# Kernel optimization log

Hardware: AMD Instinct MI355X
Metric: run time of the kernel (lower is better)

Reference implementation:

```python
import jax, jax.numpy as jnp
import numpy as np

B, C, H, W = 8, 64, 256, 256  # H must equal W (matmul shape constraint in original)


def setup_inputs() -> dict:
    key = jax.random.key(0)
    ks = jax.random.split(key, 7)
    s = 1.0 / np.sqrt(C)  # fan-in scaled init, like conv default scale
    return {
        "x": jax.random.normal(ks[0], (B, C, H, W), dtype=jnp.float32),
        "Wq": jax.random.normal(ks[1], (C, C), dtype=jnp.float32) * s,
        "bq": jax.random.normal(ks[2], (C,), dtype=jnp.float32) * s,
        "Wk": jax.random.normal(ks[3], (C, C), dtype=jnp.float32) * s,
        "bk": jax.random.normal(ks[4], (C,), dtype=jnp.float32) * s,
        "Wv": jax.random.normal(ks[5], (C, C), dtype=jnp.float32) * s,
        "bv": jax.random.normal(ks[6], (C,), dtype=jnp.float32) * s,
    }


def _conv1x1(x, Wt, b):
    # 1x1 Conv2d == per-pixel GEMM over channels: [o,c] x [b,c,h,w] -> [b,o,h,w]
    return jnp.einsum("oc,bchw->bohw", Wt, x) + b[None, :, None, None]


def reference(x, Wq, bq, Wk, bk, Wv, bv):
    q = _conv1x1(x, Wq, bq)
    k = _conv1x1(x, Wk, bk)
    v = _conv1x1(x, Wv, bv)
    # attn[b,c,i,j] = sum_h q[b,c,h,i] * k[b,c,h,j]   (q^T @ k over spatial)
    attn = jnp.einsum("bchi,bchj->bcij", q, k)
    # softmax over the CHANNEL axis (dim=-3 in torch == axis 1 here)
    attn = jax.nn.softmax(attn, axis=1)
    # out[b,c,i,j] = sum_m attn[b,c,i,m] * v[b,c,m,j]  (requires H == W)
    out = jnp.einsum("bcim,bcmj->bcij", attn, v)
    return out
```

## Files before the change

kernel.cpp:

```cpp
#include <hip/hip_runtime.h>
#include <math.h>

constexpr int CH  = 64;
constexpr int WW  = 256;
constexpr int HWS = WW * WW;
constexpr int NB  = 8;

typedef __attribute__((ext_vector_type(8))) short bf16x8;
typedef __attribute__((ext_vector_type(4))) float f32x4;

__device__ inline ushort f2bf(float f) {
    uint u = __float_as_uint(f);
    u += 0x7fffu + ((u >> 16) & 1u);
    return (ushort)(u >> 16);
}

__device__ inline uint packsplit(float f) {
    const uint fu = __float_as_uint(f);
    const float lo = f - __uint_as_float(fu & 0xffff0000u);
    return (fu & 0xffff0000u) | (__float_as_uint(lo) >> 16);
}

union FragU { uint u[4]; bf16x8 v; };

__global__ __launch_bounds__(256) void qkv_mfma(
    const float* __restrict__ x,
    const float* __restrict__ Wq, const float* __restrict__ bq,
    const float* __restrict__ Wk, const float* __restrict__ bk,
    const float* __restrict__ Wv, const float* __restrict__ bv,
    uint* __restrict__ Q, uint* __restrict__ K, ushort* __restrict__ V)
{
    __shared__ ushort Xhi[128 * 64] __attribute__((aligned(16)));
    __shared__ ushort Xlo[128 * 64] __attribute__((aligned(16)));

    const int tid  = threadIdx.x;
    const int ln   = tid & 63;
    const int wid  = tid >> 6;
    const int ml   = ln & 15;
    const int quad = ln >> 4;

    const int n0 = blockIdx.x * 128;
    const int b  = n0 >> 16;
    const int pb = n0 & 65535;
    const float* xb = x + ((size_t)(b * CH) << 16);

    bf16x8 Ah[3][2], Al[3][2];
    float biasv[3][4];
#pragma unroll
    for (int a = 0; a < 3; ++a) {
        const int mt = wid * 3 + a;
        const float* Wsrc = (mt < 4) ? Wq : (mt < 8) ? Wk : Wv;
        const float* bsrc = (mt < 4) ? bq : (mt < 8) ? bk : bv;
        const int o = (mt & 3) * 16 + ml;
#pragma unroll
        for (int kf = 0; kf < 2; ++kf) {
            FragU Hh, Ll;
#pragma unroll
            for (int rp = 0; rp < 4; ++rp) {
                const float f0 = Wsrc[o * 64 + kf * 32 + quad * 8 + rp * 2];
                const float f1 = Wsrc[o * 64 + kf * 32 + quad * 8 + rp * 2 + 1];
                const uint u0 = __float_as_uint(f0);
                const uint u1 = __float_as_uint(f1);
                const float g0 = f0 - __uint_as_float(u0 & 0xffff0000u);
                const float g1 = f1 - __uint_as_float(u1 & 0xffff0000u);
                Hh.u[rp] = __builtin_amdgcn_perm(u1, u0, 0x07060302u);
                Ll.u[rp] = __builtin_amdgcn_perm(__float_as_uint(g1),
                                                 __float_as_uint(g0), 0x07060302u);
            }
            Ah[a][kf] = Hh.v; Al[a][kf] = Ll.v;
        }
#pragma unroll
        for (int r = 0; r < 4; ++r)
            biasv[a][r] = bsrc[(mt & 3) * 16 + quad * 4 + r];
    }

#pragma unroll
    for (int p = 0; p < 8; ++p) {
        const int flat = p * 256 + tid;
        const int c    = flat >> 5;
        const int px4  = (flat & 31) * 4;
        const float4 xv = *(const float4*)&xb[((size_t)c << 16) + pb + px4];
#pragma unroll
        for (int u = 0; u < 4; ++u) {
            const int px = px4 + u;
            const float f = (&xv.x)[u];
            const uint fu = __float_as_uint(f);
            const float lo = f - __uint_as_float(fu & 0xffff0000u);
            const int adr = px * 64 + ((((c >> 3) ^ ((px >> 1) & 7))) << 3) + (c & 7);
            Xhi[adr] = (ushort)(fu >> 16);
            Xlo[adr] = (ushort)(__float_as_uint(lo) >> 16);
        }
    }
    __syncthreads();

    f32x4 acc[3][8];
    const f32x4 zero = {0.f, 0.f, 0.f, 0.f};
#pragma unroll
    for (int a = 0; a < 3; ++a)
#pragma unroll
        for (int t = 0; t < 8; ++t) acc[a][t] = zero;

#pragma unroll
    for (int t = 0; t < 8; ++t) {
        const int px = t * 16 + ml;
        bf16x8 Bh[2], Bl[2];
#pragma unroll
        for (int kf = 0; kf < 2; ++kf) {
            const int g   = kf * 4 + quad;
            const int adr = px * 64 + ((g ^ ((px >> 1) & 7)) << 3);
            Bh[kf] = *(const bf16x8*)&Xhi[adr];
            Bl[kf] = *(const bf16x8*)&Xlo[adr];
        }
#pragma unroll
        for (int a = 0; a < 3; ++a) {
#pragma unroll
            for (int kf = 0; kf < 2; ++kf) {
                acc[a][t] = __builtin_amdgcn_mfma_f32_16x16x32_bf16(Ah[a][kf], Bh[kf], acc[a][t], 0, 0, 0);
                acc[a][t] = __builtin_amdgcn_mfma_f32_16x16x32_bf16(Ah[a][kf], Bl[kf], acc[a][t], 0, 0, 0);
                acc[a][t] = __builtin_amdgcn_mfma_f32_16x16x32_bf16(Al[a][kf], Bh[kf], acc[a][t], 0, 0, 0);
            }
        }
    }

#pragma unroll
    for (int a = 0; a < 3; ++a) {
        const int mt = wid * 3 + a;
        const int ch = (mt & 3) * 16 + quad * 4;
        if (mt < 4) {
#pragma unroll
            for (int t = 0; t < 8; ++t)
#pragma unroll
                for (int r = 0; r < 4; ++r)
                    Q[((size_t)(b * CH + ch + r) << 16) + pb + t * 16 + ml] =
                        packsplit(acc[a][t][r] + biasv[a][r]);
        } else if (mt < 8) {
#pragma unroll
            for (int t = 0; t < 8; ++t)
#pragma unroll
                for (int r = 0; r < 4; ++r)
                    K[((size_t)(b * CH + ch + r) << 16) + pb + t * 16 + ml] =
                        packsplit(acc[a][t][r] + biasv[a][r]);
        } else {
#pragma unroll
            for (int t = 0; t < 8; ++t)
#pragma unroll
                for (int r = 0; r < 4; ++r)
                    V[((size_t)(b * CH + ch + r) << 16) + pb + t * 16 + ml] =
                        f2bf(acc[a][t][r] + biasv[a][r]);
        }
    }
}

__global__ __launch_bounds__(256) void attn_mfma2(
    const uint* __restrict__ Qp, const uint* __restrict__ Kp,
    float* __restrict__ attn)
{
    const int gid = blockIdx.x;
    const int bc  = gid >> 2;
    const int i0  = ((gid >> 1) & 1) * 128;
    const int j0  = (gid & 1) * 128;
    const uint* q = Qp + (size_t)bc * HWS;
    const uint* k = Kp + (size_t)bc * HWS;
    float* out    = attn + (size_t)bc * HWS;

    const int tid  = threadIdx.x;
    const int L    = tid & 63;
    const int wid  = tid >> 6;
    const int wy   = (wid >> 1) * 64;
    const int wx   = (wid & 1) * 64;
    const int ml   = L & 15;
    const int quad = L >> 4;

    const f32x4 zero = {0.f, 0.f, 0.f, 0.f};
    f32x4 acc[4][4];
#pragma unroll
    for (int a = 0; a < 4; ++a)
#pragma unroll
        for (int b = 0; b < 4; ++b) acc[a][b] = zero;

    for (int k0 = 0; k0 < WW; k0 += 32) {
        const size_t rb = (size_t)(k0 + quad * 8) * WW;
        uint ua[4][8], ub[4][8];
#pragma unroll
        for (int a = 0; a < 4; ++a) {
            const uint* p = q + rb + i0 + wy + a * 16 + ml;
#pragma unroll
            for (int j = 0; j < 8; ++j) ua[a][j] = p[j * WW];
        }
#pragma unroll
        for (int b = 0; b < 4; ++b) {
            const uint* p = k + rb + j0 + wx + b * 16 + ml;
#pragma unroll
            for (int j = 0; j < 8; ++j) ub[b][j] = p[j * WW];
        }

        bf16x8 Ahf[4], Alf[4], Bhf[4], Blf[4];
#pragma unroll
        for (int a = 0; a < 4; ++a) {
            FragU H, Lo;
#pragma unroll
            for (int rp = 0; rp < 4; ++rp) {
                H.u[rp]  = __builtin_amdgcn_perm(ua[a][rp * 2 + 1], ua[a][rp * 2], 0x07060302u);
                Lo.u[rp] = __builtin_amdgcn_perm(ua[a][rp * 2 + 1], ua[a][rp * 2], 0x05040100u);
            }
            Ahf[a] = H.v; Alf[a] = Lo.v;
        }
#pragma unroll
        for (int b = 0; b < 4; ++b) {
            FragU H, Lo;
#pragma unroll
            for (int rp = 0; rp < 4; ++rp) {
                H.u[rp]  = __builtin_amdgcn_perm(ub[b][rp * 2 + 1], ub[b][rp * 2], 0x07060302u);
                Lo.u[rp] = __builtin_amdgcn_perm(ub[b][rp * 2 + 1], ub[b][rp * 2], 0x05040100u);
            }
            Bhf[b] = H.v; Blf[b] = Lo.v;
        }

#pragma unroll
        for (int a = 0; a < 4; ++a)
#pragma unroll
            for (int b = 0; b < 4; ++b) {
                acc[a][b] = __builtin_amdgcn_mfma_f32_16x16x32_bf16(Ahf[a], Bhf[b], acc[a][b], 0, 0, 0);
                acc[a][b] = __builtin_amdgcn_mfma_f32_16x16x32_bf16(Ahf[a], Blf[b], acc[a][b], 0, 0, 0);
                acc[a][b] = __builtin_amdgcn_mfma_f32_16x16x32_bf16(Alf[a], Bhf[b], acc[a][b], 0, 0, 0);
            }
    }

#pragma unroll
    for (int a = 0; a < 4; ++a)
#pragma unroll
        for (int b = 0; b < 4; ++b)
#pragma unroll
            for (int r = 0; r < 4; ++r)
                out[(size_t)(i0 + wy + a * 16 + quad * 4 + r) * WW
                    + j0 + wx + b * 16 + ml] = acc[a][b][r];
}

__global__ __launch_bounds__(256) void transpose_v(
    const ushort* __restrict__ Vb, ushort* __restrict__ Vt)
{
    const int blk = blockIdx.x;
    const int bc  = blk >> 2;
    const int m0  = ((blk >> 1) & 1) * 128;
    const int j0  = (blk & 1) * 128;
    const ushort* src = Vb + (size_t)bc * HWS;
    ushort* dst       = Vt + (size_t)bc * HWS;

    __shared__ ushort T[128][128] __attribute__((aligned(16)));

    const int tid = threadIdx.x;
#pragma unroll
    for (int p = 0; p < 8; ++p) {
        const int id  = p * 256 + tid;
        const int mm  = id >> 4;
        const int c16 = id & 15;
        const int cg  = (c16 + (mm >> 3)) & 15;
        *(uint4*)&T[mm][cg * 8] =
            *(const uint4*)(src + (size_t)(m0 + mm) * WW + j0 + c16 * 8);
    }
    __syncthreads();
#pragma unroll
    for (int p = 0; p < 4; ++p) {
        const int id  = p * 256 + tid;
        const int c16 = id & 15;
        const int jjp = id >> 4;
        const int jj  = jjp * 2;
        const int jjg = jj >> 3;
        ushort ra[8], rb[8];
#pragma unroll
        for (int u = 0; u < 8; ++u) {
            const int mm = c16 * 8 + u;
            const int cg = (jjg + c16) & 15;
            const uint pr = *(const uint*)&T[mm][cg * 8 + (jj & 7)];
            ra[u] = (ushort)(pr & 0xffffu);
            rb[u] = (ushort)(pr >> 16);
        }
        *(uint4*)(dst + (size_t)(j0 + jj)     * WW + m0 + c16 * 8) = *(uint4*)ra;
        *(uint4*)(dst + (size_t)(j0 + jj + 1) * WW + m0 + c16 * 8) = *(uint4*)rb;
    }
}

__global__ __launch_bounds__(128) void softmax_kernel(
    const float* __restrict__ logits, ushort* __restrict__ Wb)
{
    const int gid = blockIdx.x;
    const int b   = gid >> 8;
    const int i   = gid & 255;
    const int j2  = threadIdx.x * 2;
    const size_t off = (((size_t)(b * CH)) << 16) + (size_t)i * WW + j2;
    const float* base = logits + off;
    ushort* wout      = Wb + off;

    float2 v[CH];
#pragma unroll
    for (int c = 0; c < CH; ++c) v[c] = *(const float2*)&base[((size_t)c) << 16];

    float mx = v[0].x, my = v[0].y;
#pragma unroll
    for (int c = 1; c < CH; ++c) { mx = fmaxf(mx, v[c].x); my = fmaxf(my, v[c].y); }

    float sx = 0.f, sy = 0.f;
#pragma unroll
    for (int c = 0; c < CH; ++c) {
        v[c].x = __expf(v[c].x - mx); sx += v[c].x;
        v[c].y = __expf(v[c].y - my); sy += v[c].y;
    }
    const float ix = 1.0f / sx, iy = 1.0f / sy;
#pragma unroll
    for (int c = 0; c < CH; ++c) {
        ushort2 o;
        o.x = f2bf(v[c].x * ix);
        o.y = f2bf(v[c].y * iy);
        *(ushort2*)&wout[((size_t)c) << 16] = o;
    }
}

__global__ __launch_bounds__(256) void pv_kernel2(
    const ushort* __restrict__ Wb, const ushort* __restrict__ Vt,
    float* __restrict__ out)
{
    const int blk = blockIdx.x;
    const int bc  = blk >> 2;
    const int i0  = ((blk >> 1) & 1) * 128;
    const int j0  = (blk & 1) * 128;
    const ushort* w  = Wb + (size_t)bc * HWS;
    const ushort* vt = Vt + (size_t)bc * HWS;
    float* o         = out + (size_t)bc * HWS;

    __shared__ ushort As[128][40] __attribute__((aligned(16)));
    __shared__ ushort Bs[128][40] __attribute__((aligned(16)));

    const int tid  = threadIdx.x;
    const int L    = tid & 63;
    const int wid  = tid >> 6;
    const int wy   = (wid >> 1) * 64;
    const int wx   = (wid & 1) * 64;
    const int ml   = L & 15;
    const int quad = L >> 4;

    f32x4 zero = {0.f, 0.f, 0.f, 0.f};
    f32x4 acc[4][4];
#pragma unroll
    for (int a = 0; a < 4; ++a)
#pragma unroll
        for (int b = 0; b < 4; ++b) acc[a][b] = zero;

    for (int m0 = 0; m0 < WW; m0 += 32) {
#pragma unroll
        for (int p = 0; p < 2; ++p) {
            const int id  = p * 256 + tid;
            const int row = id >> 2;
            const int c4  = id & 3;
            *(uint4*)&As[row][c4 * 8] =
                *(const uint4*)(w  + (size_t)(i0 + row) * WW + m0 + c4 * 8);
            *(uint4*)&Bs[row][c4 * 8] =
                *(const uint4*)(vt + (size_t)(j0 + row) * WW + m0 + c4 * 8);
        }
        __syncthreads();

        bf16x8 af[4], bfr[4];
#pragma unroll
        for (int t = 0; t < 4; ++t)
            af[t]  = *(const bf16x8*)&As[wy + t * 16 + ml][quad * 8];
#pragma unroll
        for (int t = 0; t < 4; ++t)
            bfr[t] = *(const bf16x8*)&Bs[wx + t * 16 + ml][quad * 8];
#pragma unroll
        for (int a = 0; a < 4; ++a)
#pragma unroll
            for (int b = 0; b < 4; ++b)
                acc[a][b] = __builtin_amdgcn_mfma_f32_16x16x32_bf16(
                    af[a], bfr[b], acc[a][b], 0, 0, 0);
        __syncthreads();
    }

#pragma unroll
    for (int a = 0; a < 4; ++a)
#pragma unroll
        for (int b = 0; b < 4; ++b)
#pragma unroll
            for (int r = 0; r < 4; ++r)
                o[(size_t)(i0 + wy + a * 16 + quad * 4 + r) * WW
                  + j0 + wx + b * 16 + ml] = acc[a][b][r];
}

extern "C" void kernel_launch(void* const* d_in, const int* in_sizes, int n_in,
                              void* d_out, int out_size, void* d_ws, size_t ws_size,
                              hipStream_t stream) {
    const float* x  = (const float*)d_in[0];
    const float* Wq = (const float*)d_in[1];
    const float* bq = (const float*)d_in[2];
    const float* Wk = (const float*)d_in[3];
    const float* bk = (const float*)d_in[4];
    const float* Wv = (const float*)d_in[5];
    const float* bv = (const float*)d_in[6];
    float* out = (float*)d_out;

    const size_t NEL = (size_t)NB * CH * HWS;
    uint*   Qp = (uint*)d_ws;
    uint*   Kp = Qp + NEL;
    ushort* Vb = (ushort*)(Kp + NEL);
    ushort* Vt = Vb + NEL;
    ushort* Wb = (ushort*)d_ws;

    qkv_mfma<<<(NB * HWS) / 128, 256, 0, stream>>>(x, Wq, bq, Wk, bk, Wv, bv, Qp, Kp, Vb);
    attn_mfma2<<<NB * CH * 4, 256, 0, stream>>>(Qp, Kp, out);
    transpose_v<<<NB * CH * 4, 256, 0, stream>>>(Vb, Vt);
    softmax_kernel<<<NB * WW, 128, 0, stream>>>(out, Wb);
    pv_kernel2<<<NB * CH * 4, 256, 0, stream>>>(Wb, Vt, out);
}
```

Baseline: 566.4 us.

## Store Q/K in h-grouped-by-8 layout so attention loads use 128-bit vectors

The QKV projection kernel now tiles over 8 rows x 16 columns of pixels and writes Q and K in a layout where the 8 consecutive h values for each column are contiguous, staging them through shared memory so each thread can emit uint4 stores. The attention kernel then loads its MFMA fragments with two 16-byte vector loads instead of eight strided 4-byte loads. This targets the uncoalesced, scalar global reads in the QK^T kernel. The cost is an extra shared-memory round trip and two more barriers in the projection kernel.

```diff
diff --git a/kernel.cpp b/kernel.cpp
--- a/kernel.cpp
+++ b/kernel.cpp
@@ -23,15 +23,16 @@
 
 union FragU { uint u[4]; bf16x8 v; };
 
-__global__ __launch_bounds__(256) void qkv_mfma(
+__global__ __launch_bounds__(256) void qkv_mfma2(
     const float* __restrict__ x,
     const float* __restrict__ Wq, const float* __restrict__ bq,
     const float* __restrict__ Wk, const float* __restrict__ bk,
     const float* __restrict__ Wv, const float* __restrict__ bv,
     uint* __restrict__ Q, uint* __restrict__ K, ushort* __restrict__ V)
 {
-    __shared__ ushort Xhi[128 * 64] __attribute__((aligned(16)));
-    __shared__ ushort Xlo[128 * 64] __attribute__((aligned(16)));
+    __shared__ uint SH[64 * 132] __attribute__((aligned(16)));
+    ushort* Xhi = (ushort*)SH;
+    ushort* Xlo = (ushort*)&SH[4096];
 
     const int tid  = threadIdx.x;
     const int ln   = tid & 63;
@@ -39,9 +40,13 @@
     const int ml   = ln & 15;
     const int quad = ln >> 4;
 
-    const int n0 = blockIdx.x * 128;
-    const int b  = n0 >> 16;
-    const int pb = n0 & 65535;
+    const int bid = blockIdx.x;
+    const int b   = bid >> 9;
+    const int rr  = bid & 511;
+    const int ht  = rr >> 4;
+    const int it  = rr & 15;
+    const int h0  = ht * 8;
+    const int i0  = it * 16;
     const float* xb = x + ((size_t)(b * CH) << 16);
 
     bf16x8 Ah[3][2], Al[3][2];
@@ -78,11 +83,13 @@
     for (int p = 0; p < 8; ++p) {
         const int flat = p * 256 + tid;
         const int c    = flat >> 5;
-        const int px4  = (flat & 31) * 4;
-        const float4 xv = *(const float4*)&xb[((size_t)c << 16) + pb + px4];
+        const int hl   = (flat >> 2) & 7;
+        const int i4   = (flat & 3) * 4;
+        const float4 xv =
+            *(const float4*)&xb[((size_t)c << 16) + (h0 + hl) * 256 + i0 + i4];
 #pragma unroll
         for (int u = 0; u < 4; ++u) {
-            const int px = px4 + u;
+            const int px = hl * 16 + i4 + u;
             const float f = (&xv.x)[u];
             const uint fu = __float_as_uint(f);
             const float lo = f - __uint_as_float(fu & 0xffff0000u);
@@ -125,33 +132,54 @@
 #pragma unroll
     for (int a = 0; a < 3; ++a) {
         const int mt = wid * 3 + a;
-        const int ch = (mt & 3) * 16 + quad * 4;
-        if (mt < 4) {
+        if (mt >= 8) {
+            const int ch = (mt & 3) * 16 + quad * 4;
 #pragma unroll
             for (int t = 0; t < 8; ++t)
 #pragma unroll
                 for (int r = 0; r < 4; ++r)
-                    Q[((size_t)(b * CH + ch + r) << 16) + pb + t * 16 + ml] =
-                        packsplit(acc[a][t][r] + biasv[a][r]);
-        } else if (mt < 8) {
+                    V[((size_t)(b * CH + ch + r) << 16) + (h0 + t) * 256 + i0 + ml] =
+                        f2bf(acc[a][t][r] + biasv[a][r]);
+        }
+    }
+
+    const int crd = tid >> 2;
+    const int ilc = (tid & 3) * 4;
+
+#pragma unroll
+    for (int mat = 0; mat < 2; ++mat) {
+        __syncthreads();
+#pragma unroll
+        for (int a = 0; a < 3; ++a) {
+            const int mt = wid * 3 + a;
+            if ((mt >> 2) == mat) {
+                const int ch = (mt & 3) * 16 + quad * 4;
+#pragma unroll
+                for (int r = 0; r < 4; ++r)
+#pragma unroll
+                    for (int t = 0; t < 8; ++t)
+                        SH[(ch + r) * 132 + ml * 8 + (t ^ (ml & 7))] =
+                            packsplit(acc[a][t][r] + biasv[a][r]);
+            }
+        }
+        __syncthreads();
+        uint* dstbase = (mat == 0) ? Q : K;
+#pragma unroll
+        for (int ii = 0; ii < 4; ++ii) {
+            const int il = ilc + ii;
+            uint tmp[8];
 #pragma unroll
             for (int t = 0; t < 8; ++t)
-#pragma unroll
-                for (int r = 0; r < 4; ++r)
-                    K[((size_t)(b * CH + ch + r) << 16) + pb + t * 16 + ml] =
-                        packsplit(acc[a][t][r] + biasv[a][r]);
-        } else {
-#pragma unroll
-            for (int t = 0; t < 8; ++t)
-#pragma unroll
-                for (int r = 0; r < 4; ++r)
-                    V[((size_t)(b * CH + ch + r) << 16) + pb + t * 16 + ml] =
-                        f2bf(acc[a][t][r] + biasv[a][r]);
-        }
-    }
-}
-
-__global__ __launch_bounds__(256) void attn_mfma2(
+                tmp[t] = SH[crd * 132 + il * 8 + (t ^ (il & 7))];
+            uint* dst = dstbase + ((size_t)(b * CH + crd) << 16)
+                        + ht * 2048 + (size_t)(i0 + il) * 8;
+            *(uint4*)dst       = *(uint4*)&tmp[0];
+            *(uint4*)(dst + 4) = *(uint4*)&tmp[4];
+        }
+    }
+}
+
+__global__ __launch_bounds__(256) void attn_mfma3(
     const uint* __restrict__ Qp, const uint* __restrict__ Kp,
     float* __restrict__ attn)
 {
@@ -179,19 +207,19 @@
         for (int b = 0; b < 4; ++b) acc[a][b] = zero;
 
     for (int k0 = 0; k0 < WW; k0 += 32) {
-        const size_t rb = (size_t)(k0 + quad * 8) * WW;
+        const size_t gb = (size_t)((k0 >> 3) + quad) * 2048;
         uint ua[4][8], ub[4][8];
 #pragma unroll
         for (int a = 0; a < 4; ++a) {
-            const uint* p = q + rb + i0 + wy + a * 16 + ml;
-#pragma unroll
-            for (int j = 0; j < 8; ++j) ua[a][j] = p[j * WW];
+            const uint* p = q + gb + (size_t)(i0 + wy + a * 16 + ml) * 8;
+            *(uint4*)&ua[a][0] = *(const uint4*)p;
+            *(uint4*)&ua[a][4] = *(const uint4*)(p + 4);
         }
 #pragma unroll
         for (int b = 0; b < 4; ++b) {
-            const uint* p = k + rb + j0 + wx + b * 16 + ml;
-#pragma unroll
-            for (int j = 0; j < 8; ++j) ub[b][j] = p[j * WW];
+            const uint* p = k + gb + (size_t)(j0 + wx + b * 16 + ml) * 8;
+            *(uint4*)&ub[b][0] = *(const uint4*)p;
+            *(uint4*)&ub[b][4] = *(const uint4*)(p + 4);
         }
 
         bf16x8 Ahf[4], Alf[4], Bhf[4], Blf[4];
@@ -403,8 +431,8 @@
     ushort* Vt = Vb + NEL;
     ushort* Wb = (ushort*)d_ws;
 
-    qkv_mfma<<<(NB * HWS) / 128, 256, 0, stream>>>(x, Wq, bq, Wk, bk, Wv, bv, Qp, Kp, Vb);
-    attn_mfma2<<<NB * CH * 4, 256, 0, stream>>>(Qp, Kp, out);
+    qkv_mfma2<<<(NB * HWS) / 128, 256, 0, stream>>>(x, Wq, bq, Wk, bk, Wv, bv, Qp, Kp, Vb);
+    attn_mfma3<<<NB * CH * 4, 256, 0, stream>>>(Qp, Kp, out);
     transpose_v<<<NB * CH * 4, 256, 0, stream>>>(Vb, Vt);
     softmax_kernel<<<NB * WW, 128, 0, stream>>>(out, Wb);
     pv_kernel2<<<NB * CH * 4, 256, 0, stream>>>(Wb, Vt, out);
```

After: 615.7 us. 1.09x slower.
